# Optimization experiments

Hardware: AMD Instinct MI355X
Metric: run time of the kernel (lower is better)

The kernel has to match this reference:

```python
import jax, jax.numpy as jnp
import numpy as np

N_HEADS, N_KV_HEADS, HEAD_DIM = 32, 8, 64
ROPE_BASE = 10000.0
NEG_INF = -1e30


def _rope_tables(t):
    inv_freq = 1.0 / (ROPE_BASE ** (jnp.arange(0, HEAD_DIM, 2, dtype=jnp.float32) / HEAD_DIM))
    ang = jnp.arange(t, dtype=jnp.float32)[:, None] * inv_freq[None, :]  # (t, hd/2)
    emb = jnp.concatenate([ang, ang], axis=-1)  # (t, hd)
    return jnp.cos(emb), jnp.sin(emb)


def _apply_rope(x, cos, sin):
    # x: (b, h, t, hd); cos/sin: (t, hd)
    x1, x2 = jnp.split(x, 2, axis=-1)
    rot = jnp.concatenate([-x2, x1], axis=-1)
    return x * cos[None, None] + rot * sin[None, None]


def setup_inputs() -> dict:
    key = jax.random.key(0)
    ks = jax.random.split(key, 5)
    b, t, d, kv = 4, 1024, 2048, 512
    s = 0.02
    return {
        'x': jax.random.normal(ks[0], (b, t, d), jnp.float32),
        'Wq': jax.random.normal(ks[1], (d, d), jnp.float32) * s,
        'Wk': jax.random.normal(ks[2], (d, kv), jnp.float32) * s,
        'Wv': jax.random.normal(ks[3], (d, kv), jnp.float32) * s,
        'Wo': jax.random.normal(ks[4], (d, d), jnp.float32) * s,
    }


def reference(x, Wq, Wk, Wv, Wo):
    b, t, d = x.shape
    g = N_HEADS // N_KV_HEADS
    scale = HEAD_DIM ** 0.5
    q = (x @ Wq).reshape(b, t, N_HEADS, HEAD_DIM).transpose(0, 2, 1, 3)
    k = (x @ Wk).reshape(b, t, N_KV_HEADS, HEAD_DIM).transpose(0, 2, 1, 3)
    v = (x @ Wv).reshape(b, t, N_KV_HEADS, HEAD_DIM).transpose(0, 2, 1, 3)
    cos, sin = _rope_tables(t)
    q = _apply_rope(q, cos, sin)
    k = _apply_rope(k, cos, sin)
    k = jnp.repeat(k, g, axis=1)  # GQA expand to (b, H, t, hd)
    v = jnp.repeat(v, g, axis=1)
    dot = jnp.einsum('bhqd,bhkd->bhqk', q, k)
    q_nsq = jnp.sum(q * q, axis=-1, keepdims=True)        # (b,H,t,1)
    k_nsq = jnp.sum(k * k, axis=-1, keepdims=True)        # (b,H,t,1)
    scores = (dot - 0.5 * q_nsq - 0.5 * jnp.swapaxes(k_nsq, -1, -2)) / scale
    causal = jnp.tril(jnp.ones((t, t), dtype=bool))
    scores = jnp.where(causal[None, None], scores, NEG_INF)
    attn = jax.nn.softmax(scores, axis=-1)
    y = jnp.einsum('bhqk,bhkd->bhqd', attn, v)
    y = y.transpose(0, 2, 1, 3).reshape(b, t, d)
    return y @ Wo
```

## Files before the change

### kernel.cpp

```cpp
#include <hip/hip_runtime.h>

typedef __bf16 bf16x8 __attribute__((ext_vector_type(8)));
typedef __bf16 bf16x4v __attribute__((ext_vector_type(4)));
typedef float f32x4 __attribute__((ext_vector_type(4)));

#define LDS_ASYNC16(g, l)                                            \
  __builtin_amdgcn_global_load_lds(                                  \
      (__attribute__((address_space(1))) void*)(g),                  \
      (__attribute__((address_space(3))) void*)(l), 16, 0, 0)

#define MFMA16(a, b, c) __builtin_amdgcn_mfma_f32_16x16x32_bf16(a, b, c, 0, 0, 0)

#if __has_builtin(__builtin_amdgcn_exp2f)
#define EXP2F(x) __builtin_amdgcn_exp2f(x)
#else
#define EXP2F(x) exp2f(x)
#endif

#define QSCALE 0.18033688011112042f
#define KBIAS -0.09016844005556021f
#define LN1E4_32 0.28782313662425572f

__global__ void cast_bf16(const float* __restrict__ x, __bf16* __restrict__ y,
                          int n4) {
  int i = blockIdx.x * 256 + threadIdx.x;
  if (i < n4) {
    float4 v = ((const float4*)x)[i];
    bf16x4v o;
    o[0] = (__bf16)v.x; o[1] = (__bf16)v.y; o[2] = (__bf16)v.z; o[3] = (__bf16)v.w;
    ((bf16x4v*)y)[i] = o;
  }
}

__global__ void wtrans_all(const float* __restrict__ Wq,
                           const float* __restrict__ Wk,
                           const float* __restrict__ Wv,
                           const float* __restrict__ Wo,
                           __bf16* __restrict__ W1T, __bf16* __restrict__ WoT) {
  __shared__ float tile[64][65];
  int gy = blockIdx.y;
  const float* src;
  int srcld, n0;
  __bf16* dst;
  if (gy < 32) {
    src = Wq; srcld = 2048; dst = W1T; n0 = gy * 64;
  } else if (gy < 40) {
    src = Wk; srcld = 512; dst = W1T + (size_t)2048 * 2048; n0 = (gy - 32) * 64;
  } else if (gy < 48) {
    src = Wv; srcld = 512; dst = W1T + (size_t)2560 * 2048; n0 = (gy - 40) * 64;
  } else {
    src = Wo; srcld = 2048; dst = WoT; n0 = (gy - 48) * 64;
  }
  int k0 = blockIdx.x * 64;
  int tl = threadIdx.x >> 6, c = threadIdx.x & 63;
#pragma unroll
  for (int rr = 0; rr < 16; ++rr) {
    int k = rr * 4 + tl;
    tile[k][c] = src[(size_t)(k0 + k) * srcld + n0 + c];
  }
  __syncthreads();
#pragma unroll
  for (int rr = 0; rr < 16; ++rr) {
    int n = rr * 4 + tl;
    dst[(size_t)(n0 + n) * 2048 + k0 + c] = (__bf16)tile[c][n];
  }
}

template <int OUTBF16>
__global__ __launch_bounds__(256) void gemm_bt(const __bf16* __restrict__ A,
                                               const __bf16* __restrict__ B,
                                               void* __restrict__ Cout, int M,
                                               int N, int K) {
  __shared__ __bf16 As[128 * 32];
  __shared__ __bf16 Bs[128 * 32];
  int tid = threadIdx.x;
  int wave = tid >> 6, lane = tid & 63;
  int quad = lane >> 4, l16 = lane & 15;
  int wm = (wave & 1) * 64, wn = (wave >> 1) * 64;
  int tm = blockIdx.y * 128, tn = blockIdx.x * 128;

  f32x4 acc[4][4] = {};

  int srow = tid >> 2;
  int scol = (tid & 3) * 8;
  const __bf16* gA = A + (size_t)(tm + srow) * K + scol;
  const __bf16* gB = B + (size_t)(tn + srow) * K + scol;
  __bf16* lA0 = As + wave * 512;
  __bf16* lA1 = As + 2048 + wave * 512;
  __bf16* lB0 = Bs + wave * 512;
  __bf16* lB1 = Bs + 2048 + wave * 512;
  size_t stepA = (size_t)64 * K;

  for (int k0 = 0; k0 < K; k0 += 32) {
    LDS_ASYNC16(gA, lA0);
    LDS_ASYNC16(gA + stepA, lA1);
    LDS_ASYNC16(gB, lB0);
    LDS_ASYNC16(gB + stepA, lB1);
    gA += 32;
    gB += 32;
    __syncthreads();
    bf16x8 af[4], bfr[4];
#pragma unroll
    for (int mt = 0; mt < 4; ++mt)
      af[mt] = *(const bf16x8*)(As + (wm + mt * 16 + l16) * 32 + quad * 8);
#pragma unroll
    for (int nt = 0; nt < 4; ++nt)
      bfr[nt] = *(const bf16x8*)(Bs + (wn + nt * 16 + l16) * 32 + quad * 8);
#pragma unroll
    for (int mt = 0; mt < 4; ++mt)
#pragma unroll
      for (int nt = 0; nt < 4; ++nt)
        acc[mt][nt] = MFMA16(af[mt], bfr[nt], acc[mt][nt]);
    __syncthreads();
  }
  int r0 = tm + wm + quad * 4;
  int c0 = tn + wn + l16;
#pragma unroll
  for (int mt = 0; mt < 4; ++mt)
#pragma unroll
    for (int nt = 0; nt < 4; ++nt)
#pragma unroll
      for (int r = 0; r < 4; ++r) {
        size_t idx = (size_t)(r0 + mt * 16 + r) * N + (c0 + nt * 16);
        if (OUTBF16)
          ((__bf16*)Cout)[idx] = (__bf16)acc[mt][nt][r];
        else
          ((float*)Cout)[idx] = acc[mt][nt][r];
      }
}

__global__ __launch_bounds__(256) void gemm_qkv(
    const __bf16* __restrict__ A, const __bf16* __restrict__ B,
    __bf16* __restrict__ Qr, __bf16* __restrict__ Kr, __bf16* __restrict__ VT,
    float* __restrict__ bias2) {
  const int K = 2048;
  __shared__ __bf16 As[128 * 32];
  __shared__ __bf16 Bs[128 * 32];
  int tid = threadIdx.x;
  int wave = tid >> 6, lane = tid & 63;
  int quad = lane >> 4, l16 = lane & 15;
  int wm = (wave & 1) * 64, wn = (wave >> 1) * 64;
  int tm = blockIdx.y * 128, tn = blockIdx.x * 128;

  f32x4 acc[4][4] = {};

  int srow = tid >> 2;
  int scol = (tid & 3) * 8;
  const __bf16* gA = A + (size_t)(tm + srow) * K + scol;
  const __bf16* gB = B + (size_t)(tn + srow) * K + scol;
  __bf16* lA0 = As + wave * 512;
  __bf16* lA1 = As + 2048 + wave * 512;
  __bf16* lB0 = Bs + wave * 512;
  __bf16* lB1 = Bs + 2048 + wave * 512;
  size_t stepA = (size_t)64 * K;

  for (int k0 = 0; k0 < K; k0 += 32) {
    LDS_ASYNC16(gA, lA0);
    LDS_ASYNC16(gA + stepA, lA1);
    LDS_ASYNC16(gB, lB0);
    LDS_ASYNC16(gB + stepA, lB1);
    gA += 32;
    gB += 32;
    __syncthreads();
    bf16x8 af[4], bfr[4];
#pragma unroll
    for (int mt = 0; mt < 4; ++mt)
      af[mt] = *(const bf16x8*)(As + (wm + mt * 16 + l16) * 32 + quad * 8);
#pragma unroll
    for (int nt = 0; nt < 4; ++nt)
      bfr[nt] = *(const bf16x8*)(Bs + (wn + nt * 16 + l16) * 32 + quad * 8);
#pragma unroll
    for (int mt = 0; mt < 4; ++mt)
#pragma unroll
      for (int nt = 0; nt < 4; ++nt)
        acc[mt][nt] = MFMA16(af[mt], bfr[nt], acc[mt][nt]);
    __syncthreads();
  }

  int r0 = tm + wm + quad * 4;
  int c0 = tn + wn;

  if (blockIdx.x < 20) {
    bool isQ = (blockIdx.x < 16);
    float invf0 = expf((float)l16 * -LN1E4_32);
    float invf1 = expf((float)(l16 + 16) * -LN1E4_32);
    int h = isQ ? (c0 >> 6) : ((c0 - 2048) >> 6);
    __bf16* base = isQ ? Qr : Kr;
    int nh = isQ ? 32 : 8;
#pragma unroll
    for (int mt = 0; mt < 4; ++mt) {
      float nsq[4];
#pragma unroll
      for (int r = 0; r < 4; ++r) {
        int row = r0 + mt * 16 + r;
        int t = row & 1023, b = row >> 10;
        float tf = (float)t;
        float a0 = tf * invf0, a1 = tf * invf1;
        float s0, c0f, s1, c1f;
        sincosf(a0, &s0, &c0f);
        sincosf(a1, &s1, &c1f);
        float oa = acc[mt][0][r] * c0f - acc[mt][2][r] * s0;
        float oc = acc[mt][2][r] * c0f + acc[mt][0][r] * s0;
        float ob = acc[mt][1][r] * c1f - acc[mt][3][r] * s1;
        float od = acc[mt][3][r] * c1f + acc[mt][1][r] * s1;
        if (isQ) {
          oa *= QSCALE; ob *= QSCALE; oc *= QSCALE; od *= QSCALE;
        }
        __bf16 ba = (__bf16)oa, bb = (__bf16)ob, bc = (__bf16)oc,
               bd = (__bf16)od;
        __bf16* dst = base + (((size_t)b * nh + h) * 1024 + t) * 64;
        dst[l16] = ba;
        dst[16 + l16] = bb;
        dst[32 + l16] = bc;
        dst[48 + l16] = bd;
        float fa = (float)ba, fb = (float)bb, fc = (float)bc, fd = (float)bd;
        nsq[r] = fa * fa + fb * fb + fc * fc + fd * fd;
      }
      if (!isQ) {
#pragma unroll
        for (int r = 0; r < 4; ++r) {
          float nl = nsq[r];
          nl += __shfl_xor(nl, 1);
          nl += __shfl_xor(nl, 2);
          nl += __shfl_xor(nl, 4);
          nl += __shfl_xor(nl, 8);
          if (l16 == 0) {
            int row = r0 + mt * 16 + r;
            int t = row & 1023, b = row >> 10;
            bias2[((size_t)b * 8 + h) * 1024 + t] = KBIAS * nl;
          }
        }
      }
    }
  } else {
    int kvh = (c0 - 2560) >> 6;
#pragma unroll
    for (int mt = 0; mt < 4; ++mt) {
      int rowb = r0 + mt * 16;
      int t = rowb & 1023, b = rowb >> 10;
#pragma unroll
      for (int nt = 0; nt < 4; ++nt) {
        int d = nt * 16 + l16;
        bf16x4v ov;
#pragma unroll
        for (int r = 0; r < 4; ++r) ov[r] = (__bf16)acc[mt][nt][r];
        *(bf16x4v*)(VT + ((size_t)(b * 8 + kvh) * 64 + d) * 1024 + t) = ov;
      }
    }
  }
}

__global__ __launch_bounds__(256, 2) void attn_kernel(
    const __bf16* __restrict__ Q, const __bf16* __restrict__ Kc,
    const __bf16* __restrict__ VT, const float* __restrict__ bias2,
    __bf16* __restrict__ Y) {
  const int T = 1024;
  int h = blockIdx.x, qt = 7 - blockIdx.y, b = blockIdx.z;
  int kv = h >> 2;
  int tid = threadIdx.x;
  int wave = tid >> 6, lane = tid & 63;
  int quad = lane >> 4, l16 = lane & 15;

  __shared__ __bf16 KsA[2][8 * 128 * 8];
  __shared__ __bf16 VsA[2][16 * 64 * 8];
  __shared__ __bf16 Ps[4][8 * 32 * 8];

  const __bf16* Qb = Q + (((size_t)b * 32 + h) * T + qt * 128 + wave * 32) * 64;
  const __bf16* Kb = Kc + ((size_t)b * 8 + kv) * T * 64;
  const __bf16* Vb = VT + ((size_t)b * 8 + kv) * 64 * T;
  const float* nb = bias2 + ((size_t)b * 8 + kv) * T;
  __bf16* Pw = &Ps[wave][0];

  bf16x8 qf[2][2];
#pragma unroll
  for (int nt = 0; nt < 2; ++nt)
#pragma unroll
    for (int kd = 0; kd < 2; ++kd)
      qf[nt][kd] =
          *(const bf16x8*)(Qb + (size_t)(nt * 16 + l16) * 64 + kd * 32 + quad * 8);

  bf16x8 onesf;
#pragma unroll
  for (int u = 0; u < 8; ++u) onesf[u] = (__bf16)1.0f;

  f32x4 oacc[2][4] = {};
  f32x4 lacc[2] = {};

#define STAGE_TILE(k0_, buf_)                                                 \
  {                                                                           \
    _Pragma("unroll") for (int u = 0; u < 8; ++u) {                           \
      int t = wave * 8 + u;                                                   \
      if (t < 16) {                                                           \
        int c = t >> 1, kh = t & 1;                                           \
        LDS_ASYNC16(                                                          \
            Kb + (size_t)((k0_) + kh * 64) * 64 + c * 8 + (size_t)lane * 64,  \
            KsA[buf_] + c * 1024 + kh * 512);                                 \
      } else {                                                                \
        int c = t - 16;                                                       \
        LDS_ASYNC16(Vb + (size_t)lane * T + (k0_) + c * 8,                    \
                    VsA[buf_] + c * 512);                                     \
      }                                                                       \
    }                                                                         \
  }

  STAGE_TILE(0, 0);

  for (int j = 0; j <= qt; ++j) {
    int k0 = j * 128;
    int cur = j & 1;
    bool diag = (j == qt);

    f32x4 bv[8];
#pragma unroll
    for (int mt = 0; mt < 8; ++mt)
      bv[mt] = *(const f32x4*)(nb + k0 + mt * 16 + quad * 4);

    if (j < qt) {
      STAGE_TILE(k0 + 128, cur ^ 1);
      asm volatile("s_waitcnt vmcnt(8)" ::: "memory");
    } else {
      asm volatile("s_waitcnt vmcnt(0)" ::: "memory");
    }
    __builtin_amdgcn_s_barrier();

    const __bf16* Ksc = KsA[cur];
    const __bf16* Vsc = VsA[cur];

    f32x4 sacc[8][2];
#pragma unroll
    for (int mt = 0; mt < 8; ++mt) {
      sacc[mt][0] = bv[mt];
      sacc[mt][1] = bv[mt];
    }
#pragma unroll
    for (int kd = 0; kd < 2; ++kd)
#pragma unroll
      for (int mt = 0; mt < 8; ++mt) {
        bf16x8 kf =
            *(const bf16x8*)(Ksc + (kd * 4 + quad) * 1024 + (mt * 16 + l16) * 8);
        sacc[mt][0] = MFMA16(kf, qf[0][kd], sacc[mt][0]);
        sacc[mt][1] = MFMA16(kf, qf[1][kd], sacc[mt][1]);
      }

    if (diag) {
#pragma unroll
      for (int mt = 0; mt < 8; ++mt)
#pragma unroll
        for (int nt = 0; nt < 2; ++nt)
#pragma unroll
          for (int r = 0; r < 4; ++r) {
            int key = mt * 16 + quad * 4 + r;
            int ql = wave * 32 + nt * 16 + l16;
            if (key > ql) sacc[mt][nt][r] = -1e30f;
          }
    }

#pragma unroll
    for (int kh = 0; kh < 2; ++kh) {
#pragma unroll
      for (int mh = 0; mh < 4; ++mh) {
        int mt = 4 * kh + mh;
        int cp = 2 * mh + (quad >> 1);
        int halfo = (quad & 1) * 4;
#pragma unroll
        for (int nt = 0; nt < 2; ++nt) {
          bf16x4v pk;
#pragma unroll
          for (int r = 0; r < 4; ++r) pk[r] = (__bf16)EXP2F(sacc[mt][nt][r]);
          int qs = ((nt * 16 + l16) + 2 * cp) & 31;
          *(bf16x4v*)(Pw + cp * 256 + qs * 8 + halfo) = pk;
        }
      }
#pragma unroll
      for (int kil = 0; kil < 2; ++kil) {
        int cp = 4 * kil + quad;
        bf16x8 pf0 = *(const bf16x8*)(Pw + cp * 256 + ((l16 + 2 * cp) & 31) * 8);
        bf16x8 pf1 =
            *(const bf16x8*)(Pw + cp * 256 + ((16 + l16 + 2 * cp) & 31) * 8);
        lacc[0] = MFMA16(onesf, pf0, lacc[0]);
        lacc[1] = MFMA16(onesf, pf1, lacc[1]);
        int s = 2 * kh + kil;
#pragma unroll
        for (int dt = 0; dt < 4; ++dt) {
          bf16x8 vf = *(const bf16x8*)(Vsc + (4 * s + quad) * 512 +
                                       (dt * 16 + l16) * 8);
          oacc[0][dt] = MFMA16(vf, pf0, oacc[0][dt]);
          oacc[1][dt] = MFMA16(vf, pf1, oacc[1][dt]);
        }
      }
    }
    __builtin_amdgcn_s_barrier();
  }

#pragma unroll
  for (int nt = 0; nt < 2; ++nt) {
    float linv = 1.0f / lacc[nt][0];
    __bf16* Yr =
        Y + (((size_t)b * T + qt * 128 + wave * 32 + nt * 16 + l16) * 32 + h) * 64;
#pragma unroll
    for (int dt = 0; dt < 4; ++dt) {
      bf16x4v ov;
#pragma unroll
      for (int r = 0; r < 4; ++r) ov[r] = (__bf16)(oacc[nt][dt][r] * linv);
      *(bf16x4v*)(Yr + dt * 16 + quad * 4) = ov;
    }
  }
#undef STAGE_TILE
}

extern "C" void kernel_launch(void* const* d_in, const int* in_sizes, int n_in,
                              void* d_out, int out_size, void* d_ws,
                              size_t ws_size, hipStream_t stream) {
  const float* x = (const float*)d_in[0];
  const float* Wq = (const float*)d_in[1];
  const float* Wk = (const float*)d_in[2];
  const float* Wv = (const float*)d_in[3];
  const float* Wo = (const float*)d_in[4];
  float* out = (float*)d_out;

  char* ws = (char*)d_ws;
  __bf16* xb = (__bf16*)(ws);
  __bf16* W1T = (__bf16*)(ws + 16777216);
  __bf16* WoT = (__bf16*)(ws + 16777216 + 12582912);
  char* d4 = ws + 16777216 + 12582912 + 8388608;
  __bf16* Qr = (__bf16*)(d4);
  __bf16* Kr = (__bf16*)(d4 + 16777216);
  __bf16* VT = (__bf16*)(d4 + 16777216 + 4194304);
  float* bias2 = (float*)(d4 + 16777216 + 8388608);
  __bf16* y = xb;

  cast_bf16<<<8192, 256, 0, stream>>>(x, xb, 2097152);
  wtrans_all<<<dim3(32, 80), 256, 0, stream>>>(Wq, Wk, Wv, Wo, W1T, WoT);
  gemm_qkv<<<dim3(24, 32), 256, 0, stream>>>(xb, W1T, Qr, Kr, VT, bias2);
  attn_kernel<<<dim3(32, 8, 4), 256, 0, stream>>>(Qr, Kr, VT, bias2, y);
  gemm_bt<0><<<dim3(16, 32), 256, 0, stream>>>(y, WoT, out, 4096, 2048, 2048);
}
```

Before: 286.4 us.

## Double-buffer GEMM LDS loads with async prefetch and merge prep kernels

Both GEMM kernels now use two LDS buffers: the next k-tile is fetched asynchronously while MFMAs run on the current one, synchronised with explicit vmcnt waits and raw s_barrier calls in place of two __syncthreads per step. The input cast and weight transpose/cast kernels are merged into a single launch through extra grid rows. This is meant to hide global load latency in the GEMM main loop and remove one kernel launch. In exchange, LDS use per block doubles, which may lower occupancy, and the hand-written waitcnt logic depends on the load count per stage being exactly right.

```diff
diff --git a/kernel.cpp b/kernel.cpp
--- a/kernel.cpp
+++ b/kernel.cpp
@@ -21,24 +21,29 @@
 #define KBIAS -0.09016844005556021f
 #define LN1E4_32 0.28782313662425572f
 
-__global__ void cast_bf16(const float* __restrict__ x, __bf16* __restrict__ y,
-                          int n4) {
-  int i = blockIdx.x * 256 + threadIdx.x;
-  if (i < n4) {
-    float4 v = ((const float4*)x)[i];
-    bf16x4v o;
-    o[0] = (__bf16)v.x; o[1] = (__bf16)v.y; o[2] = (__bf16)v.z; o[3] = (__bf16)v.w;
-    ((bf16x4v*)y)[i] = o;
-  }
-}
-
-__global__ void wtrans_all(const float* __restrict__ Wq,
-                           const float* __restrict__ Wk,
-                           const float* __restrict__ Wv,
-                           const float* __restrict__ Wo,
-                           __bf16* __restrict__ W1T, __bf16* __restrict__ WoT) {
+__global__ void prep_kernel(const float* __restrict__ x,
+                            const float* __restrict__ Wq,
+                            const float* __restrict__ Wk,
+                            const float* __restrict__ Wv,
+                            const float* __restrict__ Wo,
+                            __bf16* __restrict__ xb, __bf16* __restrict__ W1T,
+                            __bf16* __restrict__ WoT) {
+  int gy = blockIdx.y;
+  if (gy >= 80) {
+    int bid = (gy - 80) * 32 + blockIdx.x;
+    int base = bid * 2048 + threadIdx.x;
+#pragma unroll
+    for (int u = 0; u < 8; ++u) {
+      int i = base + u * 256;
+      float4 v = ((const float4*)x)[i];
+      bf16x4v o;
+      o[0] = (__bf16)v.x; o[1] = (__bf16)v.y;
+      o[2] = (__bf16)v.z; o[3] = (__bf16)v.w;
+      ((bf16x4v*)xb)[i] = o;
+    }
+    return;
+  }
   __shared__ float tile[64][65];
-  int gy = blockIdx.y;
   const float* src;
   int srcld, n0;
   __bf16* dst;
@@ -66,13 +71,52 @@
   }
 }
 
+#define GEMM_PIPELINE_LOOP(KDIM)                                              \
+  {                                                                           \
+                                               \
+    LDS_ASYNC16(gA, As + wave * 512);                                         \
+    LDS_ASYNC16(gA + stepA, As + 2048 + wave * 512);                          \
+    LDS_ASYNC16(gB, Bs + wave * 512);                                         \
+    LDS_ASYNC16(gB + stepA, Bs + 2048 + wave * 512);                          \
+    gA += 32;                                                                 \
+    gB += 32;                                                                 \
+    for (int k0 = 0; k0 < (KDIM); k0 += 32) {                                 \
+      int cur = (k0 >> 5) & 1;                                                \
+      if (k0 + 32 < (KDIM)) {                                                 \
+        __bf16* dA = As + (cur ^ 1) * 4096 + wave * 512;                      \
+        __bf16* dB = Bs + (cur ^ 1) * 4096 + wave * 512;                      \
+        LDS_ASYNC16(gA, dA);                                                  \
+        LDS_ASYNC16(gA + stepA, dA + 2048);                                   \
+        LDS_ASYNC16(gB, dB);                                                  \
+        LDS_ASYNC16(gB + stepA, dB + 2048);                                   \
+        gA += 32;                                                             \
+        gB += 32;                                                             \
+        asm volatile("s_waitcnt vmcnt(4)" ::: "memory");                      \
+      } else {                                                                \
+        asm volatile("s_waitcnt vmcnt(0)" ::: "memory");                      \
+      }                                                                       \
+      __builtin_amdgcn_s_barrier();                                           \
+      const __bf16* Ac = As + cur * 4096;                                     \
+      const __bf16* Bc = Bs + cur * 4096;                                     \
+      bf16x8 af[4], bfr[4];                                                   \
+      _Pragma("unroll") for (int mt = 0; mt < 4; ++mt) af[mt] =               \
+          *(const bf16x8*)(Ac + (wm + mt * 16 + l16) * 32 + quad * 8);        \
+      _Pragma("unroll") for (int nt = 0; nt < 4; ++nt) bfr[nt] =              \
+          *(const bf16x8*)(Bc + (wn + nt * 16 + l16) * 32 + quad * 8);        \
+      _Pragma("unroll") for (int mt = 0; mt < 4; ++mt)                        \
+          _Pragma("unroll") for (int nt = 0; nt < 4; ++nt) acc[mt][nt] =      \
+              MFMA16(af[mt], bfr[nt], acc[mt][nt]);                           \
+      __builtin_amdgcn_s_barrier();                                           \
+    }                                                                         \
+  }
+
 template <int OUTBF16>
 __global__ __launch_bounds__(256) void gemm_bt(const __bf16* __restrict__ A,
                                                const __bf16* __restrict__ B,
                                                void* __restrict__ Cout, int M,
                                                int N, int K) {
-  __shared__ __bf16 As[128 * 32];
-  __shared__ __bf16 Bs[128 * 32];
+  __shared__ __bf16 As[2 * 128 * 32];
+  __shared__ __bf16 Bs[2 * 128 * 32];
   int tid = threadIdx.x;
   int wave = tid >> 6, lane = tid & 63;
   int quad = lane >> 4, l16 = lane & 15;
@@ -85,34 +129,10 @@
   int scol = (tid & 3) * 8;
   const __bf16* gA = A + (size_t)(tm + srow) * K + scol;
   const __bf16* gB = B + (size_t)(tn + srow) * K + scol;
-  __bf16* lA0 = As + wave * 512;
-  __bf16* lA1 = As + 2048 + wave * 512;
-  __bf16* lB0 = Bs + wave * 512;
-  __bf16* lB1 = Bs + 2048 + wave * 512;
   size_t stepA = (size_t)64 * K;
 
-  for (int k0 = 0; k0 < K; k0 += 32) {
-    LDS_ASYNC16(gA, lA0);
-    LDS_ASYNC16(gA + stepA, lA1);
-    LDS_ASYNC16(gB, lB0);
-    LDS_ASYNC16(gB + stepA, lB1);
-    gA += 32;
-    gB += 32;
-    __syncthreads();
-    bf16x8 af[4], bfr[4];
-#pragma unroll
-    for (int mt = 0; mt < 4; ++mt)
-      af[mt] = *(const bf16x8*)(As + (wm + mt * 16 + l16) * 32 + quad * 8);
-#pragma unroll
-    for (int nt = 0; nt < 4; ++nt)
-      bfr[nt] = *(const bf16x8*)(Bs + (wn + nt * 16 + l16) * 32 + quad * 8);
-#pragma unroll
-    for (int mt = 0; mt < 4; ++mt)
-#pragma unroll
-      for (int nt = 0; nt < 4; ++nt)
-        acc[mt][nt] = MFMA16(af[mt], bfr[nt], acc[mt][nt]);
-    __syncthreads();
-  }
+  GEMM_PIPELINE_LOOP(K);
+
   int r0 = tm + wm + quad * 4;
   int c0 = tn + wn + l16;
 #pragma unroll
@@ -134,8 +154,8 @@
     __bf16* __restrict__ Qr, __bf16* __restrict__ Kr, __bf16* __restrict__ VT,
     float* __restrict__ bias2) {
   const int K = 2048;
-  __shared__ __bf16 As[128 * 32];
-  __shared__ __bf16 Bs[128 * 32];
+  __shared__ __bf16 As[2 * 128 * 32];
+  __shared__ __bf16 Bs[2 * 128 * 32];
   int tid = threadIdx.x;
   int wave = tid >> 6, lane = tid & 63;
   int quad = lane >> 4, l16 = lane & 15;
@@ -148,34 +168,9 @@
   int scol = (tid & 3) * 8;
   const __bf16* gA = A + (size_t)(tm + srow) * K + scol;
   const __bf16* gB = B + (size_t)(tn + srow) * K + scol;
-  __bf16* lA0 = As + wave * 512;
-  __bf16* lA1 = As + 2048 + wave * 512;
-  __bf16* lB0 = Bs + wave * 512;
-  __bf16* lB1 = Bs + 2048 + wave * 512;
   size_t stepA = (size_t)64 * K;
 
-  for (int k0 = 0; k0 < K; k0 += 32) {
-    LDS_ASYNC16(gA, lA0);
-    LDS_ASYNC16(gA + stepA, lA1);
-    LDS_ASYNC16(gB, lB0);
-    LDS_ASYNC16(gB + stepA, lB1);
-    gA += 32;
-    gB += 32;
-    __syncthreads();
-    bf16x8 af[4], bfr[4];
-#pragma unroll
-    for (int mt = 0; mt < 4; ++mt)
-      af[mt] = *(const bf16x8*)(As + (wm + mt * 16 + l16) * 32 + quad * 8);
-#pragma unroll
-    for (int nt = 0; nt < 4; ++nt)
-      bfr[nt] = *(const bf16x8*)(Bs + (wn + nt * 16 + l16) * 32 + quad * 8);
-#pragma unroll
-    for (int mt = 0; mt < 4; ++mt)
-#pragma unroll
-      for (int nt = 0; nt < 4; ++nt)
-        acc[mt][nt] = MFMA16(af[mt], bfr[nt], acc[mt][nt]);
-    __syncthreads();
-  }
+  GEMM_PIPELINE_LOOP(K);
 
   int r0 = tm + wm + quad * 4;
   int c0 = tn + wn;
@@ -429,8 +424,8 @@
   float* bias2 = (float*)(d4 + 16777216 + 8388608);
   __bf16* y = xb;
 
-  cast_bf16<<<8192, 256, 0, stream>>>(x, xb, 2097152);
-  wtrans_all<<<dim3(32, 80), 256, 0, stream>>>(Wq, Wk, Wv, Wo, W1T, WoT);
+  prep_kernel<<<dim3(32, 112), 256, 0, stream>>>(x, Wq, Wk, Wv, Wo, xb, W1T,
+                                                 WoT);
   gemm_qkv<<<dim3(24, 32), 256, 0, stream>>>(xb, W1T, Qr, Kr, VT, bias2);
   attn_kernel<<<dim3(32, 8, 4), 256, 0, stream>>>(Qr, Kr, VT, bias2, y);
   gemm_bt<0><<<dim3(16, 32), 256, 0, stream>>>(y, WoT, out, 4096, 2048, 2048);
```

Result: slower. 309.5 us (+8.1%).
